# Kernel optimization log

Measured on AMD Instinct MI355X. Metric: run time of the kernel, lower is better.

## Reference

```python
import jax, jax.numpy as jnp
import numpy as np

EPS = 1e-6
N_REP = 4  # num_heads // num_kv_heads


def _qk_norm(a):
    a32 = a.astype(jnp.float32)
    var = jnp.mean(jnp.square(a32), axis=-1, keepdims=True)
    return (a32 * jax.lax.rsqrt(var + EPS)).astype(a.dtype)


def setup_inputs() -> dict:
    key = jax.random.key(0)
    ks = jax.random.split(key, 5)
    B, Tq, C, H, D, Hkv = 2, 2048, 2048, 16, 128, 4
    s = 0.02
    return {
        "x_q": jax.random.normal(ks[0], (B, Tq, C), dtype=jnp.float32),
        "Wq": jax.random.normal(ks[1], (C, H, D), dtype=jnp.float32) * s,
        "Wk": jax.random.normal(ks[2], (C, Hkv, D), dtype=jnp.float32) * s,
        "Wv": jax.random.normal(ks[3], (C, Hkv, D), dtype=jnp.float32) * s,
        "Wo": jax.random.normal(ks[4], (H * D, C), dtype=jnp.float32) * s,
    }


def reference(x_q, Wq, Wk, Wv, Wo):
    # x_q: (B, Tq, C); self-attention (x_kv = x_q)
    B, Tq, C = x_q.shape
    D = Wq.shape[-1]
    q = jnp.einsum('btc,chd->bthd', x_q, Wq)   # (B,Tq,H,D)
    k = jnp.einsum('btc,chd->bthd', x_q, Wk)   # (B,Tq,Hkv,D)
    v = jnp.einsum('btc,chd->bthd', x_q, Wv)
    # per-head QK RMS-norm
    q = _qk_norm(q)
    k = _qk_norm(k)
    # GQA: repeat kv heads (each kv head repeated N_REP times consecutively)
    k = jnp.repeat(k, N_REP, axis=2)           # (B,Tq,H,D)
    v = jnp.repeat(v, N_REP, axis=2)
    scale = jnp.asarray(1.0 / np.sqrt(D), dtype=q.dtype)
    logits = jnp.einsum('bqhd,bkhd->bhqk', q, k) * scale
    attn = jax.nn.softmax(logits, axis=-1)
    out = jnp.einsum('bhqk,bkhd->bqhd', attn, v)
    out = out.reshape(B, Tq, -1)               # (B,Tq,H*D)
    return out @ Wo                            # (B,Tq,C)
```

## Files before the change

### kernel.cpp

```cpp
#include <hip/hip_runtime.h>

typedef __attribute__((ext_vector_type(4))) float f32x4;
typedef __attribute__((ext_vector_type(16))) float f32x16;
typedef __attribute__((ext_vector_type(8))) short bf16x8;
typedef __attribute__((ext_vector_type(4))) unsigned u32x4;

#define DEV __device__ __forceinline__

DEV unsigned short f2bf(float f) {
  unsigned u = __float_as_uint(f);
  unsigned r = (u + 0x7FFFu + ((u >> 16) & 1u)) >> 16;
  return (unsigned short)r;
}
DEV float bf2f(unsigned short h) { return __uint_as_float(((unsigned)h) << 16); }

DEV unsigned cvtpk(float lo, float hi) {
  unsigned r;
  asm("v_cvt_pk_bf16_f32 %0, %1, %2" : "=v"(r) : "v"(lo), "v"(hi));
  return r;
}
DEV bf16x8 frag4(unsigned a, unsigned b, unsigned c, unsigned d) {
  u32x4 u = {a, b, c, d};
  return __builtin_bit_cast(bf16x8, u);
}

typedef __attribute__((address_space(1))) void gas_t;
typedef __attribute__((address_space(3))) void las_t;
DEV void async16(void* lds, const void* g) {
  __builtin_amdgcn_global_load_lds((gas_t*)g, (las_t*)lds, 16, 0, 0);
}

__global__ __launch_bounds__(256)
void prep(const float* __restrict__ x, const float* __restrict__ Wq,
          const float* __restrict__ Wk, const float* __restrict__ Wv,
          const float* __restrict__ Wo, unsigned short* __restrict__ Xb,
          unsigned short* __restrict__ WqkvT, unsigned short* __restrict__ WoT) {
  const int bid = blockIdx.x, t = threadIdx.x;
  if (bid < 512) {
    int idx = bid * 256 + t;
    for (; idx < 1048576; idx += 131072) {
      const float4* p = (const float4*)(x + (size_t)idx * 8);
      float4 v0 = p[0], v1 = p[1];
      bf16x8 o;
      o[0] = (short)f2bf(v0.x); o[1] = (short)f2bf(v0.y);
      o[2] = (short)f2bf(v0.z); o[3] = (short)f2bf(v0.w);
      o[4] = (short)f2bf(v1.x); o[5] = (short)f2bf(v1.y);
      o[6] = (short)f2bf(v1.z); o[7] = (short)f2bf(v1.w);
      *(bf16x8*)(Xb + (size_t)idx * 8) = o;
    }
    return;
  }
  const float* W;
  unsigned short* Wt;
  int n0, k0, Nw;
  if (bid < 4608)      { int b2 = bid - 512;  W = Wq; Wt = WqkvT;              Nw = 2048; n0 = (b2 & 63) * 32; k0 = (b2 >> 6) * 32; }
  else if (bid < 5632) { int b2 = bid - 4608; W = Wk; Wt = WqkvT + 2048 * 2048; Nw = 512;  n0 = (b2 & 15) * 32; k0 = (b2 >> 4) * 32; }
  else if (bid < 6656) { int b2 = bid - 5632; W = Wv; Wt = WqkvT + 2560 * 2048; Nw = 512;  n0 = (b2 & 15) * 32; k0 = (b2 >> 4) * 32; }
  else                 { int b2 = bid - 6656; W = Wo; Wt = WoT;                Nw = 2048; n0 = (b2 & 63) * 32; k0 = (b2 >> 6) * 32; }
  __shared__ float tile[32][33];
  const int tx = t & 31, ty = t >> 5;
#pragma unroll
  for (int r = ty; r < 32; r += 8)
    tile[r][tx] = W[(size_t)(k0 + r) * Nw + n0 + tx];
  __syncthreads();
#pragma unroll
  for (int r = ty; r < 32; r += 8)
    Wt[(size_t)(n0 + r) * 2048 + k0 + tx] = f2bf(tile[tx][r]);
}

template <int EPI>
__global__ __launch_bounds__(256, 3)
void gemm_bt(const unsigned short* __restrict__ A, const unsigned short* __restrict__ Bt,
             int Kr, float* __restrict__ Cf, int Nr,
             unsigned short* __restrict__ Qn, unsigned short* __restrict__ Kn,
             unsigned short* __restrict__ Vt, float qscale) {
  __shared__ __align__(16) unsigned short lsA[128 * 64];
  __shared__ __align__(16) unsigned short lsB[128 * 64];
  const int t = threadIdx.x;
  const int lane = t & 63;
  const int w = t >> 6, wr = w >> 1, wc = w & 1;
  const int lo = lane & 15, hi = lane >> 4;
  const int swz = lo & 7;
  const int nwg = gridDim.x * 32;
  const int bid0 = blockIdx.y * gridDim.x + blockIdx.x;
  const int sw = (bid0 & 7) * (nwg >> 3) + (bid0 >> 3);
  const int m0 = (sw & 31) * 128, n0 = (sw >> 5) * 128;

  f32x4 acc[4][4] = {};

  for (int kt = 0; kt < Kr; kt += 64) {
#pragma unroll
    for (int j = 0; j < 4; ++j) {
      int gi = j * 256 + t;
      int rw = gi >> 3, g = (gi & 7) ^ (rw & 7);
      async16(lsA + gi * 8, A + (size_t)(m0 + rw) * Kr + kt + g * 8);
      async16(lsB + gi * 8, Bt + (size_t)(n0 + rw) * Kr + kt + g * 8);
    }
    __syncthreads();
#pragma unroll
    for (int kk = 0; kk < 2; ++kk) {
      bf16x8 af[4], bfr[4];
#pragma unroll
      for (int i = 0; i < 4; ++i) {
        af[i]  = *(const bf16x8*)&lsA[(wr * 64 + i * 16 + lo) * 64 + (((kk * 4 + hi) ^ swz) << 3)];
        bfr[i] = *(const bf16x8*)&lsB[(wc * 64 + i * 16 + lo) * 64 + (((kk * 4 + hi) ^ swz) << 3)];
      }
#pragma unroll
      for (int mi = 0; mi < 4; ++mi)
#pragma unroll
        for (int ni = 0; ni < 4; ++ni)
          acc[mi][ni] = __builtin_amdgcn_mfma_f32_16x16x32_bf16(af[mi], bfr[ni], acc[mi][ni], 0, 0, 0);
    }
    __syncthreads();
  }

  float rr[4][4];
  if (EPI == 1 && n0 < 2560) {
    const float scl = (n0 < 2048) ? qscale : 1.0f;
    float p[4][4];
#pragma unroll
    for (int mi = 0; mi < 4; ++mi)
#pragma unroll
      for (int i = 0; i < 4; ++i) {
        float s = 0.f;
#pragma unroll
        for (int ni = 0; ni < 4; ++ni) s += acc[mi][ni][i] * acc[mi][ni][i];
        p[mi][i] = s;
      }
#pragma unroll
    for (int off = 1; off < 16; off <<= 1)
#pragma unroll
      for (int mi = 0; mi < 4; ++mi)
#pragma unroll
        for (int i = 0; i < 4; ++i) p[mi][i] += __shfl_xor(p[mi][i], off, 64);
    float* red = (float*)lsA;
    if (lo == 0)
#pragma unroll
      for (int mi = 0; mi < 4; ++mi)
#pragma unroll
        for (int i = 0; i < 4; ++i)
          red[(wr * 2 + wc) * 64 + mi * 16 + hi * 4 + i] = p[mi][i];
    __syncthreads();
#pragma unroll
    for (int mi = 0; mi < 4; ++mi)
#pragma unroll
      for (int i = 0; i < 4; ++i) {
        float tot = p[mi][i] + red[(wr * 2 + (wc ^ 1)) * 64 + mi * 16 + hi * 4 + i];
        rr[mi][i] = rsqrtf(tot * (1.0f / 128.0f) + 1e-6f) * scl;
      }
  }

#pragma unroll
  for (int mi = 0; mi < 4; ++mi)
#pragma unroll
    for (int ni = 0; ni < 4; ++ni)
#pragma unroll
      for (int i = 0; i < 4; ++i) {
        int gm = m0 + wr * 64 + mi * 16 + hi * 4 + i;
        int gn = n0 + wc * 64 + ni * 16 + lo;
        float v = acc[mi][ni][i];
        if (EPI == 0) {
          Cf[(size_t)gm * Nr + gn] = v;
        } else {
          if (n0 < 2560) v *= rr[mi][i];
          unsigned short bv = f2bf(v);
          int bb = gm >> 11, tt = gm & 2047;
          if (gn < 2048) {
            int hh = gn >> 7, dd = gn & 127;
            Qn[(((size_t)bb * 16 + hh) * 2048 + tt) * 128 + dd] = bv;
          } else if (gn < 2560) {
            int g2 = gn - 2048, hh = g2 >> 7, dd = g2 & 127;
            Kn[(((size_t)bb * 4 + hh) * 2048 + tt) * 128 + dd] = bv;
          } else {
            int g2 = gn - 2560, hh = g2 >> 7, dd = g2 & 127;
            Vt[(((size_t)bb * 4 + hh) * 128 + dd) * 2048 + tt] = bv;
          }
        }
      }
}

__global__ __launch_bounds__(256, 2)
void attn(const unsigned short* __restrict__ Q, const unsigned short* __restrict__ Kk,
          const unsigned short* __restrict__ Vt, unsigned short* __restrict__ AO) {
  const int bid = blockIdx.x;
  const int bh = (bid & 7) + 8 * (bid >> 7);
  const int qx = (bid >> 3) & 15;
  const int b = bh >> 4, h = bh & 15;
  const int hkv = h >> 2;
  const int t = threadIdx.x;
  const int w = t >> 6, lane = t & 63;
  const int qi = lane & 31, h1 = lane >> 5;
  const unsigned short* Qb = Q  + (size_t)bh * 2048 * 128;
  const unsigned short* Kb = Kk + (size_t)(b * 4 + hkv) * 2048 * 128;
  const unsigned short* Vb = Vt + (size_t)(b * 4 + hkv) * 128 * 2048;
  const int q0 = qx * 128 + w * 32;

  __shared__ __align__(16) unsigned short Klds[2][64 * 128];
  __shared__ __align__(16) unsigned short Vlds[2][128 * 64];

  bf16x8 qf[8];
#pragma unroll
  for (int s = 0; s < 8; ++s)
    qf[s] = *(const bf16x8*)&Qb[(size_t)(q0 + qi) * 128 + s * 16 + h1 * 8];

  f32x16 Oc[4] = {};
  float mrow = -1e30f, srow = 0.f;

#define STAGE_KV(bufi, kt_)                                                      \
  {                                                                              \
    const unsigned short* gK = Kb + (size_t)(kt_) * 128;                         \
    const unsigned short* gV = Vb + (kt_);                                       \
    _Pragma("unroll")                                                            \
    for (int j = 0; j < 4; ++j) {                                                \
      int gi = j * 256 + t;                                                      \
      int kr = gi >> 4, kg = (gi & 15) ^ (kr & 15);                              \
      async16(&Klds[bufi][gi * 8], gK + (size_t)kr * 128 + kg * 8);              \
      int vr = gi >> 3, vg = (gi & 7) ^ (vr & 7);                                \
      async16(&Vlds[bufi][gi * 8], gV + (size_t)vr * 2048 + vg * 8);             \
    }                                                                            \
  }

  STAGE_KV(0, 0);
  __syncthreads();

  int cur = 0;
  for (int kt = 0; kt < 2048; kt += 64) {
    if (kt + 64 < 2048) STAGE_KV(cur ^ 1, kt + 64);

    const unsigned short* KL = Klds[cur];
    const unsigned short* VL = Vlds[cur];

    f32x16 S[2] = {};
    __builtin_amdgcn_s_setprio(1);
#pragma unroll
    for (int mt = 0; mt < 2; ++mt) {
      const int krow = mt * 32 + qi;
      const unsigned short* krp = KL + krow * 128;
      const int rswz = krow & 15;
#pragma unroll
      for (int s = 0; s < 8; ++s) {
        bf16x8 kf = *(const bf16x8*)(krp + (((2 * s + h1) ^ rswz) << 3));
        S[mt] = __builtin_amdgcn_mfma_f32_32x32x16_bf16(kf, qf[s], S[mt], 0, 0, 0);
      }
    }
    __builtin_amdgcn_s_setprio(0);

    float t8[8];
#pragma unroll
    for (int r = 0; r < 8; ++r)
      t8[r] = fmaxf(fmaxf(S[0][r], S[0][r + 8]), fmaxf(S[1][r], S[1][r + 8]));
#pragma unroll
    for (int r = 0; r < 4; ++r) t8[r] = fmaxf(t8[r], t8[r + 4]);
    float mx = fmaxf(fmaxf(t8[0], t8[1]), fmaxf(t8[2], t8[3]));
    mx = fmaxf(mx, __shfl_xor(mx, 32, 64));
    if (__any(mx > mrow + 8.0f)) {
      float mnew = fmaxf(mrow, mx);
      float al = __builtin_amdgcn_exp2f(mrow - mnew);
      mrow = mnew;
      srow *= al;
#pragma unroll
      for (int dt = 0; dt < 4; ++dt)
#pragma unroll
        for (int r = 0; r < 16; ++r) Oc[dt][r] *= al;
    }
#pragma unroll
    for (int mt = 0; mt < 2; ++mt)
#pragma unroll
      for (int r = 0; r < 16; ++r)
        S[mt][r] = __builtin_amdgcn_exp2f(S[mt][r] - mrow);
    float s8[8];
#pragma unroll
    for (int r = 0; r < 8; ++r)
      s8[r] = (S[0][r] + S[0][r + 8]) + (S[1][r] + S[1][r + 8]);
#pragma unroll
    for (int r = 0; r < 4; ++r) s8[r] += s8[r + 4];
    float rs = (s8[0] + s8[1]) + (s8[2] + s8[3]);
    rs += __shfl_xor(rs, 32, 64);
    srow += rs;

    __builtin_amdgcn_s_setprio(1);
#pragma unroll
    for (int mt = 0; mt < 2; ++mt) {
      unsigned wd[8];
#pragma unroll
      for (int i2 = 0; i2 < 8; ++i2) wd[i2] = cvtpk(S[mt][2 * i2], S[mt][2 * i2 + 1]);
      unsigned r0 = __shfl_xor(h1 ? wd[0] : wd[2], 32, 64);
      unsigned r1 = __shfl_xor(h1 ? wd[1] : wd[3], 32, 64);
      unsigned r2 = __shfl_xor(h1 ? wd[4] : wd[6], 32, 64);
      unsigned r3 = __shfl_xor(h1 ? wd[5] : wd[7], 32, 64);
      bf16x8 pf0 = frag4(h1 ? r0 : wd[0], h1 ? r1 : wd[1], h1 ? wd[2] : r0, h1 ? wd[3] : r1);
      bf16x8 pf1 = frag4(h1 ? r2 : wd[4], h1 ? r3 : wd[5], h1 ? wd[6] : r2, h1 ? wd[7] : r3);
#pragma unroll
      for (int dt = 0; dt < 4; ++dt) {
        const int vrow = dt * 32 + qi;
        const unsigned short* vrp = VL + vrow * 64;
        const int vswz = vrow & 7;
        bf16x8 v0 = *(const bf16x8*)(vrp + (((mt * 4 + 0 + h1) ^ vswz) << 3));
        bf16x8 v1 = *(const bf16x8*)(vrp + (((mt * 4 + 2 + h1) ^ vswz) << 3));
        Oc[dt] = __builtin_amdgcn_mfma_f32_32x32x16_bf16(v0, pf0, Oc[dt], 0, 0, 0);
        Oc[dt] = __builtin_amdgcn_mfma_f32_32x32x16_bf16(v1, pf1, Oc[dt], 0, 0, 0);
      }
    }
    __builtin_amdgcn_s_setprio(0);

    __syncthreads();
    cur ^= 1;
  }

  const float inv = 1.0f / srow;
  const size_t orow = ((size_t)(b * 2048 + q0 + qi)) * 2048 + h * 128;
#pragma unroll
  for (int dt = 0; dt < 4; ++dt)
#pragma unroll
    for (int rq = 0; rq < 4; ++rq) {
      int d0 = dt * 32 + 8 * rq + 4 * h1;
      unsigned u0 = cvtpk(Oc[dt][4 * rq + 0] * inv, Oc[dt][4 * rq + 1] * inv);
      unsigned u1 = cvtpk(Oc[dt][4 * rq + 2] * inv, Oc[dt][4 * rq + 3] * inv);
      uint2 st = {u0, u1};
      *(uint2*)((unsigned short*)AO + orow + d0) = st;
    }
}

extern "C" void kernel_launch(void* const* d_in, const int* in_sizes, int n_in,
                              void* d_out, int out_size, void* d_ws, size_t ws_size,
                              hipStream_t stream) {
  const float* x_q = (const float*)d_in[0];
  const float* Wq  = (const float*)d_in[1];
  const float* Wk  = (const float*)d_in[2];
  const float* Wv  = (const float*)d_in[3];
  const float* Wo  = (const float*)d_in[4];
  float* out = (float*)d_out;

  char* ws = (char*)d_ws;
  unsigned short* Xb    = (unsigned short*)(ws);
  unsigned short* WqkvT = (unsigned short*)(ws + 16777216);
  unsigned short* WoT   = (unsigned short*)(ws + 29360128);
  unsigned short* Qn    = (unsigned short*)(ws + 37748736);
  unsigned short* Kn    = (unsigned short*)(ws + 54525952);
  unsigned short* Vt    = (unsigned short*)(ws + 58720256);
  unsigned short* AO    = Xb;

  prep<<<10752, 256, 0, stream>>>(x_q, Wq, Wk, Wv, Wo, Xb, WqkvT, WoT);

  gemm_bt<1><<<dim3(3072 / 128, 4096 / 128), 256, 0, stream>>>(Xb, WqkvT, 2048, nullptr, 0,
                                                               Qn, Kn, Vt, 0.12751742f);
  attn<<<512, 256, 0, stream>>>(Qn, Kn, Vt, AO);
  gemm_bt<0><<<dim3(2048 / 128, 4096 / 128), 256, 0, stream>>>(AO, WoT, 2048, out, 2048,
                                                               nullptr, nullptr, nullptr, 0.f);
}
```

Before: 214.3 us.

## Split attention over two KV halves with pre-fragmented V and combine pass

Adds a split-KV attention path: each query block processes half of the key sequence, doubling the grid to 1024 blocks, and writes partial outputs plus per-row max/sum. A separate combine kernel merges the two halves. V is first rearranged into MFMA-fragment order so it can be loaded straight from global memory into registers, without LDS staging. The aim is higher occupancy and a shorter per-block critical path, at the cost of extra kernel launches and extra global traffic for the partials and the V re-layout. The path is used only when the workspace is large enough.

New measurement: 694.7 us. +224.2%, slower.

```diff
diff --git a/kernel.cpp b/kernel.cpp
--- a/kernel.cpp
+++ b/kernel.cpp
@@ -179,6 +179,20 @@
       }
 }
 
+__global__ __launch_bounds__(256)
+void fragV(const unsigned short* __restrict__ Vt, unsigned short* __restrict__ Vf) {
+  int tid = blockIdx.x * 256 + threadIdx.x;
+  int bhkv = tid >> 15, c = tid & 32767;
+  int lane = c & 63, tile = c >> 10, mid = (c >> 6) & 15;
+  int dt = mid >> 2, g2 = mid & 3;
+  int d = dt * 32 + (lane & 31);
+  int g = g2 * 2 + (lane >> 5);
+  int k0 = tile * 64 + g * 8;
+  const uint4* src = (const uint4*)(Vt + ((size_t)bhkv * 128 + d) * 2048 + k0);
+  uint4* dst = (uint4*)(Vf + (size_t)bhkv * 262144 + (size_t)c * 8);
+  *dst = *src;
+}
+
 __global__ __launch_bounds__(256, 2)
 void attn(const unsigned short* __restrict__ Q, const unsigned short* __restrict__ Kk,
           const unsigned short* __restrict__ Vt, unsigned short* __restrict__ AO) {
@@ -321,6 +335,186 @@
     }
 }
 
+__global__ __launch_bounds__(256, 4)
+void attn_split(const unsigned short* __restrict__ Q, const unsigned short* __restrict__ Kk,
+                const unsigned short* __restrict__ Vf, unsigned short* __restrict__ pA,
+                unsigned short* __restrict__ pB, float* __restrict__ ms) {
+  const int bid = blockIdx.x;
+  const int x = bid & 7, r = bid >> 3;
+  const int half = r & 1, h2 = (r >> 1) & 3, qx = r >> 3;
+  const int b = x >> 2, hkv = x & 3;
+  const int h = hkv * 4 + h2, bh = b * 16 + h, bhkv = b * 4 + hkv;
+  const int t = threadIdx.x;
+  const int w = t >> 6, lane = t & 63;
+  const int qi = lane & 31, h1 = lane >> 5;
+  const unsigned short* Qb = Q  + (size_t)bh * 2048 * 128;
+  const unsigned short* Kb = Kk + (size_t)bhkv * 2048 * 128;
+  const unsigned short* Vfb = Vf + (size_t)bhkv * 262144;
+  const int q0 = qx * 128 + w * 32;
+  const int t0 = half * 16, t1 = t0 + 16;
+
+  __shared__ __align__(16) unsigned short Klds[2][64 * 128];
+
+  bf16x8 qf[8];
+#pragma unroll
+  for (int s = 0; s < 8; ++s)
+    qf[s] = *(const bf16x8*)&Qb[(size_t)(q0 + qi) * 128 + s * 16 + h1 * 8];
+
+  f32x16 Oc[4] = {};
+  float mrow = -1e30f, srow = 0.f;
+
+#define STAGE_K2(bufi, kt_)                                                      \
+  {                                                                              \
+    const unsigned short* gK = Kb + (size_t)(kt_) * 128;                         \
+    _Pragma("unroll")                                                            \
+    for (int j = 0; j < 4; ++j) {                                                \
+      int gi = j * 256 + t;                                                      \
+      int kr = gi >> 4, kg = (gi & 15) ^ (kr & 15);                              \
+      async16(&Klds[bufi][gi * 8], gK + (size_t)kr * 128 + kg * 8);              \
+    }                                                                            \
+  }
+
+  STAGE_K2(0, t0 * 64);
+  __syncthreads();
+
+  int cur = 0;
+  for (int ti = t0; ti < t1; ++ti) {
+    if (ti + 1 < t1) STAGE_K2(cur ^ 1, (ti + 1) * 64);
+
+    bf16x8 vf0[2][4], vf1[2][4];
+#pragma unroll
+    for (int mt = 0; mt < 2; ++mt)
+#pragma unroll
+      for (int dt = 0; dt < 4; ++dt) {
+        const unsigned short* vp = Vfb + ((size_t)((ti * 4 + dt) * 4 + mt * 2)) * 512 + lane * 8;
+        vf0[mt][dt] = *(const bf16x8*)(vp);
+        vf1[mt][dt] = *(const bf16x8*)(vp + 512);
+      }
+
+    const unsigned short* KL = Klds[cur];
+
+    f32x16 S[2] = {};
+    __builtin_amdgcn_s_setprio(1);
+#pragma unroll
+    for (int mt = 0; mt < 2; ++mt) {
+      const int krow = mt * 32 + qi;
+      const unsigned short* krp = KL + krow * 128;
+      const int rswz = krow & 15;
+#pragma unroll
+      for (int s = 0; s < 8; ++s) {
+        bf16x8 kf = *(const bf16x8*)(krp + (((2 * s + h1) ^ rswz) << 3));
+        S[mt] = __builtin_amdgcn_mfma_f32_32x32x16_bf16(kf, qf[s], S[mt], 0, 0, 0);
+      }
+    }
+    __builtin_amdgcn_s_setprio(0);
+
+    float t8[8];
+#pragma unroll
+    for (int r2 = 0; r2 < 8; ++r2)
+      t8[r2] = fmaxf(fmaxf(S[0][r2], S[0][r2 + 8]), fmaxf(S[1][r2], S[1][r2 + 8]));
+#pragma unroll
+    for (int r2 = 0; r2 < 4; ++r2) t8[r2] = fmaxf(t8[r2], t8[r2 + 4]);
+    float mx = fmaxf(fmaxf(t8[0], t8[1]), fmaxf(t8[2], t8[3]));
+    mx = fmaxf(mx, __shfl_xor(mx, 32, 64));
+    if (__any(mx > mrow + 8.0f)) {
+      float mnew = fmaxf(mrow, mx);
+      float al = __builtin_amdgcn_exp2f(mrow - mnew);
+      mrow = mnew;
+      srow *= al;
+#pragma unroll
+      for (int dt = 0; dt < 4; ++dt)
+#pragma unroll
+        for (int r2 = 0; r2 < 16; ++r2) Oc[dt][r2] *= al;
+    }
+#pragma unroll
+    for (int mt = 0; mt < 2; ++mt)
+#pragma unroll
+      for (int r2 = 0; r2 < 16; ++r2)
+        S[mt][r2] = __builtin_amdgcn_exp2f(S[mt][r2] - mrow);
+    float s8[8];
+#pragma unroll
+    for (int r2 = 0; r2 < 8; ++r2)
+      s8[r2] = (S[0][r2] + S[0][r2 + 8]) + (S[1][r2] + S[1][r2 + 8]);
+#pragma unroll
+    for (int r2 = 0; r2 < 4; ++r2) s8[r2] += s8[r2 + 4];
+    float rs = (s8[0] + s8[1]) + (s8[2] + s8[3]);
+    rs += __shfl_xor(rs, 32, 64);
+    srow += rs;
+
+    __builtin_amdgcn_s_setprio(1);
+#pragma unroll
+    for (int mt = 0; mt < 2; ++mt) {
+      unsigned wd[8];
+#pragma unroll
+      for (int i2 = 0; i2 < 8; ++i2) wd[i2] = cvtpk(S[mt][2 * i2], S[mt][2 * i2 + 1]);
+      unsigned r0 = __shfl_xor(h1 ? wd[0] : wd[2], 32, 64);
+      unsigned r1 = __shfl_xor(h1 ? wd[1] : wd[3], 32, 64);
+      unsigned r2_ = __shfl_xor(h1 ? wd[4] : wd[6], 32, 64);
+      unsigned r3 = __shfl_xor(h1 ? wd[5] : wd[7], 32, 64);
+      bf16x8 pf0 = frag4(h1 ? r0 : wd[0], h1 ? r1 : wd[1], h1 ? wd[2] : r0, h1 ? wd[3] : r1);
+      bf16x8 pf1 = frag4(h1 ? r2_ : wd[4], h1 ? r3 : wd[5], h1 ? wd[6] : r2_, h1 ? wd[7] : r3);
+#pragma unroll
+      for (int dt = 0; dt < 4; ++dt) {
+        Oc[dt] = __builtin_amdgcn_mfma_f32_32x32x16_bf16(vf0[mt][dt], pf0, Oc[dt], 0, 0, 0);
+        Oc[dt] = __builtin_amdgcn_mfma_f32_32x32x16_bf16(vf1[mt][dt], pf1, Oc[dt], 0, 0, 0);
+      }
+    }
+    __builtin_amdgcn_s_setprio(0);
+
+    __syncthreads();
+    cur ^= 1;
+  }
+
+  unsigned short* dst = half ? pB : pA;
+  const float inv = 1.0f / srow;
+  const size_t orow = ((size_t)(b * 2048 + q0 + qi)) * 2048 + h * 128;
+#pragma unroll
+  for (int dt = 0; dt < 4; ++dt)
+#pragma unroll
+    for (int rq = 0; rq < 4; ++rq) {
+      int d0 = dt * 32 + 8 * rq + 4 * h1;
+      unsigned u0 = cvtpk(Oc[dt][4 * rq + 0] * inv, Oc[dt][4 * rq + 1] * inv);
+      unsigned u1 = cvtpk(Oc[dt][4 * rq + 2] * inv, Oc[dt][4 * rq + 3] * inv);
+      uint2 st = {u0, u1};
+      *(uint2*)(dst + orow + d0) = st;
+    }
+  if (h1 == 0) {
+    int rowg = (bh << 11) + q0 + qi;
+    ms[((size_t)half * 65536 + rowg) * 2 + 0] = mrow;
+    ms[((size_t)half * 65536 + rowg) * 2 + 1] = srow;
+  }
+}
+
+__global__ __launch_bounds__(256)
+void combine(unsigned short* __restrict__ pA, const unsigned short* __restrict__ pB,
+             const float* __restrict__ ms) {
+  int tid = blockIdx.x * 256 + threadIdx.x;
+  int r2 = tid >> 8;
+  int rest = tid & 255;
+  int h = rest >> 4, c8 = rest & 15;
+  int bb = r2 >> 11, tt = r2 & 2047;
+  int rowm = ((bb * 16 + h) << 11) + tt;
+  float ma = ms[(size_t)rowm * 2 + 0], sa = ms[(size_t)rowm * 2 + 1];
+  float mb = ms[((size_t)65536 + rowm) * 2 + 0], sb = ms[((size_t)65536 + rowm) * 2 + 1];
+  float M = fmaxf(ma, mb);
+  float wa = sa * __builtin_amdgcn_exp2f(ma - M);
+  float wb = sb * __builtin_amdgcn_exp2f(mb - M);
+  float inv = 1.0f / (wa + wb);
+  wa *= inv; wb *= inv;
+  size_t addr = (size_t)r2 * 2048 + h * 128 + c8 * 8;
+  bf16x8 a = *(const bf16x8*)(pA + addr);
+  bf16x8 b = *(const bf16x8*)(pB + addr);
+  unsigned o[4];
+#pragma unroll
+  for (int i = 0; i < 4; ++i) {
+    float f0 = wa * bf2f((unsigned short)a[2 * i])     + wb * bf2f((unsigned short)b[2 * i]);
+    float f1 = wa * bf2f((unsigned short)a[2 * i + 1]) + wb * bf2f((unsigned short)b[2 * i + 1]);
+    o[i] = cvtpk(f0, f1);
+  }
+  u32x4 ov = {o[0], o[1], o[2], o[3]};
+  *(u32x4*)(pA + addr) = ov;
+}
+
 extern "C" void kernel_launch(void* const* d_in, const int* in_sizes, int n_in,
                               void* d_out, int out_size, void* d_ws, size_t ws_size,
                               hipStream_t stream) {
@@ -339,12 +533,21 @@
   unsigned short* Kn    = (unsigned short*)(ws + 54525952);
   unsigned short* Vt    = (unsigned short*)(ws + 58720256);
   unsigned short* AO    = Xb;
+  unsigned short* Vf    = WqkvT;
+  unsigned short* pB    = (unsigned short*)(ws + 62914560);
+  float*          ms    = (float*)(ws + 79691776);
+  const bool split = ws_size >= 80740352ull;
 
   prep<<<10752, 256, 0, stream>>>(x_q, Wq, Wk, Wv, Wo, Xb, WqkvT, WoT);
-
   gemm_bt<1><<<dim3(3072 / 128, 4096 / 128), 256, 0, stream>>>(Xb, WqkvT, 2048, nullptr, 0,
                                                                Qn, Kn, Vt, 0.12751742f);
-  attn<<<512, 256, 0, stream>>>(Qn, Kn, Vt, AO);
+  if (split) {
+    fragV<<<1024, 256, 0, stream>>>(Vt, Vf);
+    attn_split<<<1024, 256, 0, stream>>>(Qn, Kn, Vf, AO, pB, ms);
+    combine<<<4096, 256, 0, stream>>>(AO, pB, ms);
+  } else {
+    attn<<<512, 256, 0, stream>>>(Qn, Kn, Vt, AO);
+  }
   gemm_bt<0><<<dim3(2048 / 128, 4096 / 128), 256, 0, stream>>>(AO, WoT, 2048, out, 2048,
                                                                nullptr, nullptr, nullptr, 0.f);
 }
```
